# Kernel optimization log

Measured on AMD Instinct MI355X. Metric: run time of the kernel, lower is better.

Reference implementation:

```python
import jax, jax.numpy as jnp
import numpy as np

D_MODEL = 1024
N_HEADS = 16
D_K = D_MODEL // N_HEADS
D_FF = 4096
LN_EPS = 1e-5


def _layer_norm(x, gamma, beta):
    mu = jnp.mean(x, axis=-1, keepdims=True)
    var = jnp.mean(jnp.square(x - mu), axis=-1, keepdims=True)
    return (x - mu) * jax.lax.rsqrt(var + LN_EPS) * gamma + beta


def setup_inputs() -> dict:
    key = jax.random.key(0)
    ks = jax.random.split(key, 16)
    B, S = 2, 2048
    x = jax.random.normal(ks[0], (B, S, D_MODEL), dtype=jnp.float32)
    # causal mask: True = masked (as used by masked_fill)
    mask = ~jnp.tril(jnp.ones((S, S), dtype=bool))
    s = 1.0 / np.sqrt(D_MODEL)
    sf = 1.0 / np.sqrt(D_FF)
    inp = {
        "x": x,
        "mask": mask,
        "ln1_g": jnp.ones((D_MODEL,), jnp.float32),
        "ln1_b": jnp.zeros((D_MODEL,), jnp.float32),
        "ln2_g": jnp.ones((D_MODEL,), jnp.float32),
        "ln2_b": jnp.zeros((D_MODEL,), jnp.float32),
        "Wq": jax.random.normal(ks[1], (D_MODEL, D_MODEL), jnp.float32) * s,
        "bq": jax.random.normal(ks[2], (D_MODEL,), jnp.float32) * s,
        "Wk": jax.random.normal(ks[3], (D_MODEL, D_MODEL), jnp.float32) * s,
        "bk": jax.random.normal(ks[4], (D_MODEL,), jnp.float32) * s,
        "Wv": jax.random.normal(ks[5], (D_MODEL, D_MODEL), jnp.float32) * s,
        "bv": jax.random.normal(ks[6], (D_MODEL,), jnp.float32) * s,
        "Wo": jax.random.normal(ks[7], (D_MODEL, D_MODEL), jnp.float32) * s,
        "bo": jax.random.normal(ks[8], (D_MODEL,), jnp.float32) * s,
        "W1": jax.random.normal(ks[9], (D_MODEL, D_FF), jnp.float32) * s,
        "b1": jax.random.normal(ks[10], (D_FF,), jnp.float32) * s,
        "W2": jax.random.normal(ks[11], (D_FF, D_MODEL), jnp.float32) * sf,
        "b2": jax.random.normal(ks[12], (D_MODEL,), jnp.float32) * sf,
    }
    return inp


def reference(x, mask, ln1_g, ln1_b, ln2_g, ln2_b,
              Wq, bq, Wk, bk, Wv, bv, Wo, bo, W1, b1, W2, b2):
    B, S, _ = x.shape
    normed = _layer_norm(x, ln1_g, ln1_b)
    # project and split heads: [B, H, S, Dk]
    def split_heads(t):
        return t.reshape(B, S, N_HEADS, D_K).transpose(0, 2, 1, 3)
    Q = split_heads(normed @ Wq + bq)
    K = split_heads(normed @ Wk + bk)
    V = split_heads(normed @ Wv + bv)
    qk = jnp.einsum("bhsd,bhtd->bhst", Q, K)  # [B, H, S, S]
    qk = jnp.where(mask, -jnp.inf, qk)  # mask applied BEFORE scaling, as in source
    attn = jax.nn.softmax(qk / np.sqrt(D_K), axis=-1)
    attn_out = jnp.einsum("bhst,bhtd->bhsd", attn, V)
    attn_out = attn_out.transpose(0, 2, 1, 3).reshape(B, S, D_MODEL)
    attn_out = attn_out @ Wo + bo
    res = attn_out + x  # dropout_p=0 (eval)
    h = _layer_norm(res, ln2_g, ln2_b)
    h = jax.nn.gelu(h @ W1 + b1, approximate=False)
    h = h @ W2 + b2
    return res + h
```

## Files before the change

kernel.cpp:

```cpp
#include <hip/hip_runtime.h>


typedef __bf16 bf16;
typedef __bf16 bf16x8 __attribute__((ext_vector_type(8)));
typedef float f32x4 __attribute__((ext_vector_type(4)));

#define NROWS 4096
#define DM 1024
#define SEQ 2048
#define NHEAD 16
#define DKH 64
#define DFF 4096
#define QSCALE 0.18033688f

#define GLL16(gptr, lptr) \
  __builtin_amdgcn_global_load_lds((const __attribute__((address_space(1))) void*)(gptr), \
                                   (__attribute__((address_space(3))) void*)(lptr), 16, 0, 0)

static char* g_scratch = nullptr;
namespace {
struct ScratchInit {
  ScratchInit() {
    void* p = nullptr;
    if (hipMalloc(&p, (size_t)128 * 1024 * 1024) == hipSuccess) g_scratch = (char*)p;
  }
};
static ScratchInit g_scratch_init;
}

__global__ __launch_bounds__(256) void ln_kernel(const float* __restrict__ inp,
                                                 const float* __restrict__ gamma,
                                                 const float* __restrict__ beta,
                                                 bf16* __restrict__ out) {
  int row = blockIdx.x;
  int t = threadIdx.x;
  float4 xv = *((const float4*)(inp + (size_t)row * DM) + t);
  float v[4] = {xv.x, xv.y, xv.z, xv.w};
  float s = 0.f, sq = 0.f;
#pragma unroll
  for (int i = 0; i < 4; i++) { s += v[i]; sq += v[i] * v[i]; }
#pragma unroll
  for (int m = 32; m >= 1; m >>= 1) { s += __shfl_xor(s, m); sq += __shfl_xor(sq, m); }
  __shared__ float rs[4], rq[4];
  int w = t >> 6, lane = t & 63;
  if (lane == 0) { rs[w] = s; rq[w] = sq; }
  __syncthreads();
  s = rs[0] + rs[1] + rs[2] + rs[3];
  sq = rq[0] + rq[1] + rq[2] + rq[3];
  float mu = s * (1.f / DM);
  float var = sq * (1.f / DM) - mu * mu;
  float rinv = rsqrtf(var + 1e-5f);
  float4 gv = *((const float4*)gamma + t);
  float4 bv = *((const float4*)beta + t);
  float g[4] = {gv.x, gv.y, gv.z, gv.w}, b[4] = {bv.x, bv.y, bv.z, bv.w};
  bf16 ov[4];
#pragma unroll
  for (int i = 0; i < 4; i++) ov[i] = (bf16)((v[i] - mu) * rinv * g[i] + b[i]);
  *(uint2*)(out + (size_t)row * DM + t * 4) = *(uint2*)ov;
}

__global__ __launch_bounds__(256) void concat_bias(const float* __restrict__ bq,
                                                   const float* __restrict__ bk,
                                                   const float* __restrict__ bv,
                                                   float* __restrict__ cat) {
  int i = blockIdx.x * 256 + threadIdx.x;
  float v = (i < 1024) ? bq[i] : (i < 2048 ? bk[i - 1024] : bv[i - 2048]);
  cat[i] = v;
}

__global__ __launch_bounds__(1024) void transpose_f32_bf16(const float* __restrict__ in,
                                                           bf16* __restrict__ out,
                                                           int R, int C) {
  __shared__ bf16 tile[32][33];
  int x = blockIdx.x * 32 + threadIdx.x;
  int y = blockIdx.y * 32 + threadIdx.y;
  tile[threadIdx.y][threadIdx.x] = (bf16)in[(size_t)y * C + x];
  __syncthreads();
  int ox = blockIdx.y * 32 + threadIdx.x;
  int oy = blockIdx.x * 32 + threadIdx.y;
  out[(size_t)oy * R + ox] = tile[threadIdx.x][threadIdx.y];
}

__global__ __launch_bounds__(1024) void transpose_bf16(const bf16* __restrict__ in,
                                                       bf16* __restrict__ out,
                                                       int R, int C) {
  __shared__ bf16 tile[32][33];
  size_t zoff = (size_t)blockIdx.z * (size_t)R * (size_t)C;
  int x = blockIdx.x * 32 + threadIdx.x;
  int y = blockIdx.y * 32 + threadIdx.y;
  tile[threadIdx.y][threadIdx.x] = in[zoff + (size_t)y * C + x];
  __syncthreads();
  int ox = blockIdx.y * 32 + threadIdx.x;
  int oy = blockIdx.x * 32 + threadIdx.y;
  out[zoff + (size_t)oy * R + ox] = tile[threadIdx.x][threadIdx.y];
}

#define BM 128
#define BK 64

#define EPI_QKV3 0
#define EPI_ATTN_RES 1
#define EPI_GELU 2
#define EPI_FFN2 3

template<int EPI, int BNT>
__global__ __launch_bounds__(256, 2) void gemm_bt(
    const bf16* __restrict__ A, const bf16* __restrict__ Bt,
    const float* __restrict__ bias, int Kd, int N,
    bf16* __restrict__ outb, float* __restrict__ outf,
    const float* __restrict__ add) {
  constexpr int MS = (BNT == 128) ? 4 : 2;
  __shared__ bf16 As[BM * BK];
  __shared__ bf16 Bs[BNT * BK];
  int t = threadIdx.x;
  int m0 = blockIdx.y * BM, n0 = blockIdx.x * BNT;
  int w = t >> 6, lane = t & 63, ln = lane & 15, quad = lane >> 4;
  int wm = (BNT == 128) ? (w >> 1) * 64 : w * 32;
  int wn = (BNT == 128) ? (w & 1) * 64 : 0;
  f32x4 acc[MS][4];
#pragma unroll
  for (int i = 0; i < MS; i++)
#pragma unroll
    for (int j = 0; j < 4; j++) acc[i][j] = (f32x4){0.f, 0.f, 0.f, 0.f};

  int lr = (t >> 3) & 7, lc = t & 7;
  int gcol = ((lc ^ lr) * 8);
  const bf16* Ab = A + (size_t)(m0 + w * 8 + lr) * Kd + gcol;
  const bf16* Bb = Bt + (size_t)(n0 + w * 8 + lr) * Kd + gcol;
  bf16* AsW = As + (w * 8) * BK;
  bf16* BsW = Bs + (w * 8) * BK;

  for (int k0 = 0; k0 < Kd; k0 += BK) {
    __syncthreads();
#pragma unroll
    for (int j = 0; j < 4; j++)
      GLL16(Ab + (size_t)(32 * j) * Kd + k0, AsW + 32 * j * BK);
#pragma unroll
    for (int j = 0; j < BNT / 32; j++)
      GLL16(Bb + (size_t)(32 * j) * Kd + k0, BsW + 32 * j * BK);
    __syncthreads();
#pragma unroll
    for (int kk = 0; kk < 2; kk++) {
      bf16x8 af[MS], bfr[4];
#pragma unroll
      for (int ms = 0; ms < MS; ms++) {
        int r = wm + ms * 16 + ln;
        af[ms] = *(const bf16x8*)(As + r * BK + (((kk * 4 + quad) ^ (r & 7)) * 8));
      }
#pragma unroll
      for (int ns = 0; ns < 4; ns++) {
        int r = wn + ns * 16 + ln;
        bfr[ns] = *(const bf16x8*)(Bs + r * BK + (((kk * 4 + quad) ^ (r & 7)) * 8));
      }
#pragma unroll
      for (int ms = 0; ms < MS; ms++)
#pragma unroll
        for (int ns = 0; ns < 4; ns++)
          acc[ms][ns] = __builtin_amdgcn_mfma_f32_16x16x32_bf16(af[ms], bfr[ns], acc[ms][ns], 0, 0, 0);
    }
  }

#pragma unroll
  for (int ms = 0; ms < MS; ms++) {
#pragma unroll
    for (int ns = 0; ns < 4; ns++) {
      int col = n0 + wn + ns * 16 + ln;
      float bv = bias[col];
#pragma unroll
      for (int r = 0; r < 4; r++) {
        int row = m0 + wm + ms * 16 + quad * 4 + r;
        float val = acc[ms][ns][r] + bv;
        if (EPI == EPI_QKV3) {
          int which = col >> 10, cc = col & 1023;
          int h = cc >> 6, dk = cc & 63;
          float sc = (which == 0) ? QSCALE : 1.f;
          int b = row >> 11, sx = row & 2047;
          outb[(size_t)which * (4 << 20) +
               ((((size_t)b * NHEAD + h) * SEQ) + sx) * DKH + dk] = (bf16)(val * sc);
        } else if (EPI == EPI_ATTN_RES) {
          size_t idx = (size_t)row * DM + col;
          outf[idx] = val + add[idx];
        } else if (EPI == EPI_GELU) {
          float gl = 0.5f * val * (1.f + erff(val * 0.7071067811865475f));
          outb[(size_t)row * N + col] = (bf16)gl;
        } else {
          size_t idx = (size_t)row * DM + col;
          outf[idx] = val + add[idx];
        }
      }
    }
  }
}

#define LSTR 72

__global__ __launch_bounds__(64) void attn_kernel(
    const bf16* __restrict__ Q, const bf16* __restrict__ K,
    const bf16* __restrict__ Vt, bf16* __restrict__ out) {
  __shared__ bf16 Pl[32 * LSTR];
  int bh = blockIdx.x;
  int qq = 63 - (int)blockIdx.y;
  int t = threadIdx.x, ln = t & 15, quad = t >> 4;
  int qbase = qq * 32;
  size_t bhS = (size_t)bh * SEQ;
  const bf16* Vg0 = Vt + (size_t)bh * DKH * SEQ;

  bf16x8 qa[2][2];
#pragma unroll
  for (int m = 0; m < 2; m++)
#pragma unroll
    for (int ks = 0; ks < 2; ks++)
      qa[m][ks] = *(const bf16x8*)(Q + (bhS + qbase + m * 16 + ln) * DKH + ks * 32 + quad * 8);

  bf16x8 ones;
#pragma unroll
  for (int i = 0; i < 8; i++) ones[i] = (bf16)1.0f;

  f32x4 o[2][4];
#pragma unroll
  for (int m = 0; m < 2; m++)
#pragma unroll
    for (int i = 0; i < 4; i++) o[m][i] = (f32x4){0.f, 0.f, 0.f, 0.f};
  f32x4 accl[2] = {(f32x4){0.f, 0.f, 0.f, 0.f}, (f32x4){0.f, 0.f, 0.f, 0.f}};

  int ktmax = qq >> 1;
  for (int kt = 0; kt <= ktmax; kt++) {
    const bf16* Kg = K + (bhS + kt * 64) * DKH;
    bf16x8 kbf[8], vbf[8];
#pragma unroll
    for (int ns = 0; ns < 4; ns++)
#pragma unroll
      for (int ks = 0; ks < 2; ks++)
        kbf[ns * 2 + ks] = *(const bf16x8*)(Kg + (ns * 16 + ln) * DKH + ks * 32 + quad * 8);
#pragma unroll
    for (int ns = 0; ns < 4; ns++)
#pragma unroll
      for (int ks = 0; ks < 2; ks++)
        vbf[ns * 2 + ks] = *(const bf16x8*)(Vg0 + (size_t)(ns * 16 + ln) * SEQ + kt * 64 + ks * 32 + quad * 8);

    f32x4 s[2][4];
#pragma unroll
    for (int m = 0; m < 2; m++)
#pragma unroll
      for (int ns = 0; ns < 4; ns++) s[m][ns] = (f32x4){0.f, 0.f, 0.f, 0.f};
#pragma unroll
    for (int ns = 0; ns < 4; ns++)
#pragma unroll
      for (int m = 0; m < 2; m++) {
        s[m][ns] = __builtin_amdgcn_mfma_f32_16x16x32_bf16(qa[m][0], kbf[ns * 2], s[m][ns], 0, 0, 0);
        s[m][ns] = __builtin_amdgcn_mfma_f32_16x16x32_bf16(qa[m][1], kbf[ns * 2 + 1], s[m][ns], 0, 0, 0);
      }
    if (kt == ktmax) {
#pragma unroll
      for (int m = 0; m < 2; m++)
#pragma unroll
        for (int ns = 0; ns < 4; ns++)
#pragma unroll
          for (int r = 0; r < 4; r++) {
            int qrow = qbase + m * 16 + quad * 4 + r;
            int kpos = kt * 64 + ns * 16 + ln;
            if (kpos > qrow) s[m][ns][r] = -30000.f;
          }
    }
#pragma unroll
    for (int m = 0; m < 2; m++)
#pragma unroll
      for (int ns = 0; ns < 4; ns++)
#pragma unroll
        for (int r = 0; r < 4; r++)
          Pl[(m * 16 + quad * 4 + r) * LSTR + ns * 16 + ln] =
              (bf16)__builtin_amdgcn_exp2f(s[m][ns][r]);
    bf16x8 pa[2][2];
#pragma unroll
    for (int m = 0; m < 2; m++) {
      pa[m][0] = *(const bf16x8*)(Pl + (m * 16 + ln) * LSTR + quad * 8);
      pa[m][1] = *(const bf16x8*)(Pl + (m * 16 + ln) * LSTR + 32 + quad * 8);
    }
#pragma unroll
    for (int m = 0; m < 2; m++) {
      accl[m] = __builtin_amdgcn_mfma_f32_16x16x32_bf16(pa[m][0], ones, accl[m], 0, 0, 0);
      accl[m] = __builtin_amdgcn_mfma_f32_16x16x32_bf16(pa[m][1], ones, accl[m], 0, 0, 0);
    }
#pragma unroll
    for (int ns2 = 0; ns2 < 4; ns2++)
#pragma unroll
      for (int m = 0; m < 2; m++) {
        o[m][ns2] = __builtin_amdgcn_mfma_f32_16x16x32_bf16(pa[m][0], vbf[ns2 * 2], o[m][ns2], 0, 0, 0);
        o[m][ns2] = __builtin_amdgcn_mfma_f32_16x16x32_bf16(pa[m][1], vbf[ns2 * 2 + 1], o[m][ns2], 0, 0, 0);
      }
  }

  int b = bh >> 4, h = bh & 15;
#pragma unroll
  for (int m = 0; m < 2; m++)
#pragma unroll
    for (int r = 0; r < 4; r++) {
      int sabs = qbase + m * 16 + quad * 4 + r;
      float inv = 1.f / accl[m][r];
#pragma unroll
      for (int ns2 = 0; ns2 < 4; ns2++) {
        int col = h * DKH + ns2 * 16 + ln;
        out[((size_t)b * SEQ + sabs) * DM + col] = (bf16)(o[m][ns2][r] * inv);
      }
    }
}

extern "C" void kernel_launch(void* const* d_in, const int* in_sizes, int n_in,
                              void* d_out, int out_size, void* d_ws, size_t ws_size,
                              hipStream_t stream) {
  const float* x    = (const float*)d_in[0];
  const float* ln1g = (const float*)d_in[2];
  const float* ln1b = (const float*)d_in[3];
  const float* ln2g = (const float*)d_in[4];
  const float* ln2b = (const float*)d_in[5];
  const float* Wq = (const float*)d_in[6];   const float* bq = (const float*)d_in[7];
  const float* Wk = (const float*)d_in[8];   const float* bk = (const float*)d_in[9];
  const float* Wv = (const float*)d_in[10];  const float* bv = (const float*)d_in[11];
  const float* Wo = (const float*)d_in[12];  const float* bo = (const float*)d_in[13];
  const float* W1 = (const float*)d_in[14];  const float* b1 = (const float*)d_in[15];
  const float* W2 = (const float*)d_in[16];  const float* b2 = (const float*)d_in[17];
  float* outp = (float*)d_out;

  char* scratch = g_scratch ? g_scratch : (char*)d_ws;

  bf16* Wqt = (bf16*)scratch;
  bf16* Wkt = Wqt + (1 << 20);
  bf16* Wvt = Wkt + (1 << 20);
  bf16* Wot = Wvt + (1 << 20);
  bf16* W1t = Wot + (1 << 20);
  bf16* W2t = W1t + (4 << 20);
  bf16* normed = W2t + (4 << 20);
  bf16* Qb = normed + (4 << 20);
  bf16* Kb = Qb + (4 << 20);
  bf16* Vb = Kb + (4 << 20);
  bf16* Vtb = Vb + (4 << 20);
  bf16* attn_o = Vtb + (4 << 20);
  float* resf = (float*)(attn_o + (4 << 20));
  float* bias_cat = resf + (4 << 20);
  bf16* h1 = Qb;

  dim3 b256(256), b1k(32, 32);

  ln_kernel<<<NROWS, b256, 0, stream>>>(x, ln1g, ln1b, normed);
  concat_bias<<<12, b256, 0, stream>>>(bq, bk, bv, bias_cat);

  transpose_f32_bf16<<<dim3(32, 32), b1k, 0, stream>>>(Wq, Wqt, 1024, 1024);
  transpose_f32_bf16<<<dim3(32, 32), b1k, 0, stream>>>(Wk, Wkt, 1024, 1024);
  transpose_f32_bf16<<<dim3(32, 32), b1k, 0, stream>>>(Wv, Wvt, 1024, 1024);
  transpose_f32_bf16<<<dim3(32, 32), b1k, 0, stream>>>(Wo, Wot, 1024, 1024);
  transpose_f32_bf16<<<dim3(128, 32), b1k, 0, stream>>>(W1, W1t, 1024, 4096);
  transpose_f32_bf16<<<dim3(32, 128), b1k, 0, stream>>>(W2, W2t, 4096, 1024);

  gemm_bt<EPI_QKV3, 128><<<dim3(24, 32), b256, 0, stream>>>(
      normed, Wqt, bias_cat, 1024, 3072, Qb, nullptr, nullptr);

  transpose_bf16<<<dim3(2, 64, 32), b1k, 0, stream>>>(Vb, Vtb, 2048, 64);

  attn_kernel<<<dim3(32, 64), dim3(64), 0, stream>>>(Qb, Kb, Vtb, attn_o);

  gemm_bt<EPI_ATTN_RES, 64><<<dim3(16, 32), b256, 0, stream>>>(
      attn_o, Wot, bo, 1024, 1024, nullptr, resf, x);

  ln_kernel<<<NROWS, b256, 0, stream>>>(resf, ln2g, ln2b, normed);

  gemm_bt<EPI_GELU, 128><<<dim3(32, 32), b256, 0, stream>>>(
      normed, W1t, b1, 1024, 4096, h1, nullptr, nullptr);

  gemm_bt<EPI_FFN2, 64><<<dim3(16, 32), b256, 0, stream>>>(
      h1, W2t, b2, 4096, 1024, nullptr, outp, resf);
}
```

Measured before the change: 422.9 us.

## Split attention key loop across four waves with shared-memory reduction

The attention kernel now runs 256 threads per block. Each of four wavefronts handles every fourth key tile for the same 32-query block, and the partial outputs and row sums are combined through shared memory at the end. This cuts the serial per-block key loop, which was long for late query blocks, and adds parallelism at the cost of more LDS, two barriers and a reduction step. The kernel uses no running max, so the partial sums can be added directly. The final store also becomes a vectorised 16-byte write per thread.

New measurement: 400.8 us. -5.2%, faster.

```diff
diff --git a/kernel.cpp b/kernel.cpp
--- a/kernel.cpp
+++ b/kernel.cpp
@@ -193,17 +193,19 @@
 }
 
 #define LSTR 72
-
-__global__ __launch_bounds__(64) void attn_kernel(
+#define OSTR 68
+
+__global__ __launch_bounds__(256) void attn_kernel(
     const bf16* __restrict__ Q, const bf16* __restrict__ K,
     const bf16* __restrict__ Vt, bf16* __restrict__ out) {
-  __shared__ bf16 Pl[32 * LSTR];
+  __shared__ float smem[4 * 32 * OSTR + 128];
   int bh = blockIdx.x;
   int qq = 63 - (int)blockIdx.y;
-  int t = threadIdx.x, ln = t & 15, quad = t >> 4;
+  int t = threadIdx.x, w = t >> 6, lane = t & 63, ln = lane & 15, quad = lane >> 4;
   int qbase = qq * 32;
   size_t bhS = (size_t)bh * SEQ;
   const bf16* Vg0 = Vt + (size_t)bh * DKH * SEQ;
+  bf16* Pw = (bf16*)smem + w * 32 * LSTR;
 
   bf16x8 qa[2][2];
 #pragma unroll
@@ -224,7 +226,7 @@
   f32x4 accl[2] = {(f32x4){0.f, 0.f, 0.f, 0.f}, (f32x4){0.f, 0.f, 0.f, 0.f}};
 
   int ktmax = qq >> 1;
-  for (int kt = 0; kt <= ktmax; kt++) {
+  for (int kt = w; kt <= ktmax; kt += 4) {
     const bf16* Kg = K + (bhS + kt * 64) * DKH;
     bf16x8 kbf[8], vbf[8];
 #pragma unroll
@@ -268,13 +270,13 @@
       for (int ns = 0; ns < 4; ns++)
 #pragma unroll
         for (int r = 0; r < 4; r++)
-          Pl[(m * 16 + quad * 4 + r) * LSTR + ns * 16 + ln] =
+          Pw[(m * 16 + quad * 4 + r) * LSTR + ns * 16 + ln] =
               (bf16)__builtin_amdgcn_exp2f(s[m][ns][r]);
     bf16x8 pa[2][2];
 #pragma unroll
     for (int m = 0; m < 2; m++) {
-      pa[m][0] = *(const bf16x8*)(Pl + (m * 16 + ln) * LSTR + quad * 8);
-      pa[m][1] = *(const bf16x8*)(Pl + (m * 16 + ln) * LSTR + 32 + quad * 8);
+      pa[m][0] = *(const bf16x8*)(Pw + (m * 16 + ln) * LSTR + quad * 8);
+      pa[m][1] = *(const bf16x8*)(Pw + (m * 16 + ln) * LSTR + 32 + quad * 8);
     }
 #pragma unroll
     for (int m = 0; m < 2; m++) {
@@ -290,19 +292,35 @@
       }
   }
 
+  __syncthreads();
+  float* Ob = smem;
+  float* Lb = smem + 4 * 32 * OSTR;
+#pragma unroll
+  for (int m = 0; m < 2; m++) {
+#pragma unroll
+    for (int ns2 = 0; ns2 < 4; ns2++)
+#pragma unroll
+      for (int r = 0; r < 4; r++)
+        Ob[(w * 32 + m * 16 + quad * 4 + r) * OSTR + ns2 * 16 + ln] = o[m][ns2][r];
+    if (ln == 0) {
+#pragma unroll
+      for (int r = 0; r < 4; r++) Lb[w * 32 + m * 16 + quad * 4 + r] = accl[m][r];
+    }
+  }
+  __syncthreads();
+
+  int r = t >> 3, c0 = (t & 7) * 8;
+  float l = Lb[r] + Lb[32 + r] + Lb[64 + r] + Lb[96 + r];
+  float inv = 1.f / l;
+  bf16 ov[8];
+#pragma unroll
+  for (int j = 0; j < 8; j++) {
+    float v = Ob[r * OSTR + c0 + j] + Ob[(32 + r) * OSTR + c0 + j] +
+              Ob[(64 + r) * OSTR + c0 + j] + Ob[(96 + r) * OSTR + c0 + j];
+    ov[j] = (bf16)(v * inv);
+  }
   int b = bh >> 4, h = bh & 15;
-#pragma unroll
-  for (int m = 0; m < 2; m++)
-#pragma unroll
-    for (int r = 0; r < 4; r++) {
-      int sabs = qbase + m * 16 + quad * 4 + r;
-      float inv = 1.f / accl[m][r];
-#pragma unroll
-      for (int ns2 = 0; ns2 < 4; ns2++) {
-        int col = h * DKH + ns2 * 16 + ln;
-        out[((size_t)b * SEQ + sabs) * DM + col] = (bf16)(o[m][ns2][r] * inv);
-      }
-    }
+  *(uint4*)(out + ((size_t)b * SEQ + qbase + r) * DM + h * DKH + c0) = *(uint4*)ov;
 }
 
 extern "C" void kernel_launch(void* const* d_in, const int* in_sizes, int n_in,
@@ -356,7 +374,7 @@
 
   transpose_bf16<<<dim3(2, 64, 32), b1k, 0, stream>>>(Vb, Vtb, 2048, 64);
 
-  attn_kernel<<<dim3(32, 64), dim3(64), 0, stream>>>(Qb, Kb, Vtb, attn_o);
+  attn_kernel<<<dim3(32, 64), b256, 0, stream>>>(Qb, Kb, Vtb, attn_o);
 
   gemm_bt<EPI_ATTN_RES, 64><<<dim3(16, 32), b256, 0, stream>>>(
       attn_o, Wot, bo, 1024, 1024, nullptr, resf, x);
```
